# Performance work log

Hardware: AMD Instinct MI355X
Metric: run time of the kernel (lower is better)

The kernel has to match this reference:

```python
import jax, jax.numpy as jnp
import numpy as np

# Dims: lifted grid is N_X x N_Y, input signal has N_IN dims (= N_X*N_Y).
N_X, N_Y, N_IN = 32, 32, 1024
FILT = 33              # resolution-filter taps (odd, centered)
SIGMA0 = 0.1           # resolution_filter_initial_sigma (step 0 of decay schedule)
EPS = 1e-7


def _resolution_filter(sigma):
    # Gaussian taps on normalized coords in ~[-1, 1], normalized to sum 1.
    t = (jnp.arange(FILT, dtype=jnp.float32) - FILT // 2) * (2.0 / FILT)
    k = jnp.exp(-0.5 * jnp.square(t / sigma))
    return k / jnp.sum(k)


def _interpolate_lifting_map(lm_raw, filt):
    # Circular 1-D convolution of the generator parametrization with the
    # Gaussian resolution filter along the input-signal axis.
    P = N_X * N_Y
    pad = FILT // 2
    v = lm_raw.reshape(P, 1, N_IN)
    v = jnp.concatenate([v[..., -pad:], v, v[..., :pad]], axis=-1)  # wrap pad
    k = filt.reshape(1, 1, FILT)
    out = jax.lax.conv_general_dilated(
        v, k, window_strides=(1,), padding='VALID',
        dimension_numbers=('NCH', 'OIH', 'NCH'))
    return out.reshape(N_X, N_Y, N_IN)


def setup_inputs() -> dict:
    key = jax.random.key(0)
    k1, k2 = jax.random.split(key)
    x = jax.random.normal(k1, (16384, N_IN), dtype=jnp.float32)
    lm_raw = jax.random.normal(k2, (N_X, N_Y, N_IN), dtype=jnp.float32) / np.float32(np.sqrt(N_IN))
    return {"x": x, "lm_raw": lm_raw}


def reference(x, lm_raw):
    # _demean_and_normalize_input: per-sample demean + std-normalize.
    mu = jnp.mean(x, axis=-1, keepdims=True)
    sd = jnp.std(x, axis=-1, keepdims=True)
    xn = (x - mu) / (sd + EPS)
    # _sample_resolution_filter + _interpolate_lifting_map
    filt = _resolution_filter(jnp.asarray(SIGMA0, dtype=jnp.float32))
    lm = _interpolate_lifting_map(lm_raw, filt)  # [n_x, n_y, n_in]
    # _lift: y[b, i, j] = sum_n lm[i, j, n] * x[b, n]
    y = jnp.einsum('xyn,bn->bxy', lm, xn)
    return y
```

## Files before the change

### kernel.cpp

```cpp
#include <hip/hip_runtime.h>
#include <hip/hip_bf16.h>

#define N_IN   1024
#define N_P    1024
#define FILT   33
#define PAD    16

typedef __attribute__((ext_vector_type(8))) __bf16 bf16x8;
typedef __attribute__((ext_vector_type(4))) float  f32x4;

#define GLB(p) ((const __attribute__((address_space(1))) unsigned int*)(p))
#define LDSP(p) ((__attribute__((address_space(3))) unsigned int*)(p))

__device__ __forceinline__ unsigned short f2bf(float f) {
    union { __hip_bfloat16 h; unsigned short u; } cv;
    cv.h = __float2bfloat16(f);
    return cv.u;
}

__global__ __launch_bounds__(256)
void normalize_kernel(const float* __restrict__ x, __hip_bfloat16* __restrict__ xn)
{
    const int lane = threadIdx.x & 63;
    const int row  = blockIdx.x * 4 + (threadIdx.x >> 6);

    const float4* xr = reinterpret_cast<const float4*>(x + (size_t)row * N_IN);
    float4 v[4];
    float s = 0.f, s2 = 0.f;
#pragma unroll
    for (int i = 0; i < 4; i++) {
        v[i] = xr[i * 64 + lane];
        s  += v[i].x + v[i].y + v[i].z + v[i].w;
        s2 += v[i].x * v[i].x + v[i].y * v[i].y + v[i].z * v[i].z + v[i].w * v[i].w;
    }
#pragma unroll
    for (int off = 32; off > 0; off >>= 1) {
        s  += __shfl_xor(s,  off, 64);
        s2 += __shfl_xor(s2, off, 64);
    }
    const float mu  = s * (1.0f / N_IN);
    const float var = fmaxf(s2 * (1.0f / N_IN) - mu * mu, 0.0f);
    const float inv = 1.0f / (sqrtf(var) + 1e-7f);

    ushort4* outv = reinterpret_cast<ushort4*>(xn + (size_t)row * N_IN);
#pragma unroll
    for (int i = 0; i < 4; i++) {
        ushort4 o;
        o.x = f2bf((v[i].x - mu) * inv);
        o.y = f2bf((v[i].y - mu) * inv);
        o.z = f2bf((v[i].z - mu) * inv);
        o.w = f2bf((v[i].w - mu) * inv);
        outv[i * 64 + lane] = o;
    }
}

__global__ __launch_bounds__(256)
void conv_kernel(const float* __restrict__ lm_raw, __hip_bfloat16* __restrict__ lm)
{
    __shared__ float row[N_IN];
    __shared__ float fw[FILT];
    const int tid = threadIdx.x;
    const int p   = blockIdx.x;

    if (tid < FILT) {
        float t = (tid - PAD) * (2.0f / FILT);
        float u = t * 10.0f;
        fw[tid] = expf(-0.5f * u * u);
    }
    reinterpret_cast<float4*>(row)[tid] =
        reinterpret_cast<const float4*>(lm_raw + (size_t)p * N_IN)[tid];
    __syncthreads();

    float fsum = 0.f;
#pragma unroll
    for (int f = 0; f < FILT; f++) fsum += fw[f];
    const float inv = 1.0f / fsum;

    const int n0 = tid * 4;
    float o[4] = {0.f, 0.f, 0.f, 0.f};
#pragma unroll
    for (int f = 0; f < FILT; f++) {
        const float w = fw[f];
#pragma unroll
        for (int j = 0; j < 4; j++)
            o[j] += w * row[(n0 + j + f - PAD) & (N_IN - 1)];
    }
    ushort4 ov;
    ov.x = f2bf(o[0] * inv);
    ov.y = f2bf(o[1] * inv);
    ov.z = f2bf(o[2] * inv);
    ov.w = f2bf(o[3] * inv);
    reinterpret_cast<ushort4*>(lm + (size_t)p * N_IN)[tid] = ov;
}

__global__ __launch_bounds__(512, 2)
void gemm_big(const __hip_bfloat16* __restrict__ A,
              const __hip_bfloat16* __restrict__ B,
              float* __restrict__ C,
              int M, int N, int K)
{
    constexpr int BK = 32;
    __shared__ char smem[3][32768];

    const int tid = threadIdx.x;
    const int l   = tid & 63;
    const int w   = tid >> 6;
    const int wm  = w >> 2;
    const int wn  = w & 3;

    const int o    = blockIdx.x;
    const int lin  = (o & 7) * (gridDim.x >> 3) + (o >> 3);
    const int tn   = lin & 3;
    const int tm   = lin >> 2;
    const size_t bm = (size_t)tm * 256;
    const size_t bn = (size_t)tn * 256;

    const int srow = w * 16 + (l >> 2);
    const int scol = 16 * ((l & 3) ^ ((l >> 3) & 3));
    const char* gA = (const char*)(A + (bm + srow) * (size_t)K) + scol;
    const char* gB = (const char*)(B + (bn + srow) * (size_t)K) + scol;
    const size_t rowstep = (size_t)128 * K * 2;

#define STAGE(t, b) do {                                                        \
    const char* a0_ = gA + (size_t)(t) * (BK * 2);                              \
    const char* b0_ = gB + (size_t)(t) * (BK * 2);                              \
    char* La_ = &smem[(b)][0]     + w * 1024;                                   \
    char* Lb_ = &smem[(b)][16384] + w * 1024;                                   \
    __builtin_amdgcn_global_load_lds(GLB(a0_),           LDSP(La_),        16, 0, 0); \
    __builtin_amdgcn_global_load_lds(GLB(a0_ + rowstep), LDSP(La_ + 8192), 16, 0, 0); \
    __builtin_amdgcn_global_load_lds(GLB(b0_),           LDSP(Lb_),        16, 0, 0); \
    __builtin_amdgcn_global_load_lds(GLB(b0_ + rowstep), LDSP(Lb_ + 8192), 16, 0, 0); \
} while (0)

    const int lr = l & 15;
    const int kb = l >> 4;
    const int rslot = 16 * (kb ^ ((lr >> 1) & 3));
    const int abase = (wm * 128 + lr) * 64 + rslot;
    const int bbase = 16384 + (wn * 64 + lr) * 64 + rslot;

    f32x4 acc[8][4] = {};
    const int NT = K / BK;

    STAGE(0, 0);
    STAGE(1, 1);

    int buf = 0;
    for (int t = 0; t < NT; ++t) {
        asm volatile("s_waitcnt lgkmcnt(0)" ::: "memory");
        if (t < NT - 1) asm volatile("s_waitcnt vmcnt(4)" ::: "memory");
        else            asm volatile("s_waitcnt vmcnt(0)" ::: "memory");
        __builtin_amdgcn_s_barrier();
        __builtin_amdgcn_sched_barrier(0);

        {
            const int t2 = t + 2;
            if (t2 < NT) {
                int b2 = buf + 2; if (b2 >= 3) b2 -= 3;
                STAGE(t2, b2);
            }
        }

        const char* Sb = &smem[buf][0];
        bf16x8 bfr[4], afr[4], afr2[4];
#pragma unroll
        for (int n = 0; n < 4; n++) bfr[n]  = *(const bf16x8*)(Sb + bbase + n * 1024);
#pragma unroll
        for (int m = 0; m < 4; m++) afr[m]  = *(const bf16x8*)(Sb + abase + m * 1024);

        __builtin_amdgcn_s_setprio(1);
#pragma unroll
        for (int m = 0; m < 4; m++)
#pragma unroll
            for (int n = 0; n < 4; n++)
                acc[m][n] = __builtin_amdgcn_mfma_f32_16x16x32_bf16(afr[m], bfr[n], acc[m][n], 0, 0, 0);
        __builtin_amdgcn_s_setprio(0);

#pragma unroll
        for (int m = 0; m < 4; m++) afr2[m] = *(const bf16x8*)(Sb + abase + (m + 4) * 1024);

        __builtin_amdgcn_s_setprio(1);
#pragma unroll
        for (int m = 0; m < 4; m++)
#pragma unroll
            for (int n = 0; n < 4; n++)
                acc[m + 4][n] = __builtin_amdgcn_mfma_f32_16x16x32_bf16(afr2[m], bfr[n], acc[m + 4][n], 0, 0, 0);
        __builtin_amdgcn_s_setprio(0);

        if (++buf == 3) buf = 0;
    }
#undef STAGE

    const int crow = (l >> 4) * 4;
    const int ccol = l & 15;
#pragma unroll
    for (int m = 0; m < 8; m++)
#pragma unroll
        for (int n = 0; n < 4; n++) {
#pragma unroll
            for (int r = 0; r < 4; r++) {
                const size_t row = bm + wm * 128 + m * 16 + crow + r;
                const size_t col = bn + wn * 64 + n * 16 + ccol;
                C[row * N + col] = acc[m][n][r];
            }
        }
}

extern "C" void kernel_launch(void* const* d_in, const int* in_sizes, int n_in,
                              void* d_out, int out_size, void* d_ws, size_t ws_size,
                              hipStream_t stream) {
    const float* x      = (const float*)d_in[0];
    const float* lm_raw = (const float*)d_in[1];
    float* out = (float*)d_out;

    const int M = in_sizes[0] / N_IN;

    __hip_bfloat16* xn = (__hip_bfloat16*)d_ws;
    __hip_bfloat16* lm = (__hip_bfloat16*)((char*)d_ws + (size_t)M * N_IN * 2);

    normalize_kernel<<<M / 4, 256, 0, stream>>>(x, xn);
    conv_kernel<<<N_P, 256, 0, stream>>>(lm_raw, lm);

    const int nblk = (M / 256) * (N_P / 256);
    gemm_big<<<nblk, dim3(512), 0, stream>>>(xn, lm, out, M, N_P, N_IN);
}
```

Baseline: 64.65 us.

## Restructure GEMM into 8-phase schedule with BK=64 double-buffered LDS

```diff
diff --git a/kernel.cpp b/kernel.cpp
--- a/kernel.cpp
+++ b/kernel.cpp
@@ -94,13 +94,12 @@
 }
 
 __global__ __launch_bounds__(512, 2)
-void gemm_big(const __hip_bfloat16* __restrict__ A,
+void gemm_8ph(const __hip_bfloat16* __restrict__ A,
               const __hip_bfloat16* __restrict__ B,
               float* __restrict__ C,
               int M, int N, int K)
 {
-    constexpr int BK = 32;
-    __shared__ char smem[3][32768];
+    __shared__ char smem[2][65536];
 
     const int tid = threadIdx.x;
     const int l   = tid & 63;
@@ -115,80 +114,110 @@
     const size_t bm = (size_t)tm * 256;
     const size_t bn = (size_t)tn * 256;
 
-    const int srow = w * 16 + (l >> 2);
-    const int scol = 16 * ((l & 3) ^ ((l >> 3) & 3));
+    const int srow = tid >> 3;
+    const int scol = 16 * ((tid & 7) ^ (srow & 7));
     const char* gA = (const char*)(A + (bm + srow) * (size_t)K) + scol;
     const char* gB = (const char*)(B + (bn + srow) * (size_t)K) + scol;
-    const size_t rowstep = (size_t)128 * K * 2;
-
-#define STAGE(t, b) do {                                                        \
-    const char* a0_ = gA + (size_t)(t) * (BK * 2);                              \
-    const char* b0_ = gB + (size_t)(t) * (BK * 2);                              \
-    char* La_ = &smem[(b)][0]     + w * 1024;                                   \
-    char* Lb_ = &smem[(b)][16384] + w * 1024;                                   \
-    __builtin_amdgcn_global_load_lds(GLB(a0_),           LDSP(La_),        16, 0, 0); \
-    __builtin_amdgcn_global_load_lds(GLB(a0_ + rowstep), LDSP(La_ + 8192), 16, 0, 0); \
-    __builtin_amdgcn_global_load_lds(GLB(b0_),           LDSP(Lb_),        16, 0, 0); \
-    __builtin_amdgcn_global_load_lds(GLB(b0_ + rowstep), LDSP(Lb_ + 8192), 16, 0, 0); \
+    const size_t rowstep = (size_t)64 * K * 2;
+
+#define STAGE8(kt, b) do {                                                            \
+    const char* a_ = gA + (size_t)(kt) * 128;                                         \
+    const char* b_ = gB + (size_t)(kt) * 128;                                         \
+    char* La_ = &smem[(b)][0]     + tid * 16;                                         \
+    char* Lb_ = &smem[(b)][32768] + tid * 16;                                         \
+    __builtin_amdgcn_global_load_lds(GLB(a_),               LDSP(La_),         16, 0, 0); \
+    __builtin_amdgcn_global_load_lds(GLB(a_ + rowstep),     LDSP(La_ + 8192),  16, 0, 0); \
+    __builtin_amdgcn_global_load_lds(GLB(a_ + 2 * rowstep), LDSP(La_ + 16384), 16, 0, 0); \
+    __builtin_amdgcn_global_load_lds(GLB(a_ + 3 * rowstep), LDSP(La_ + 24576), 16, 0, 0); \
+    __builtin_amdgcn_global_load_lds(GLB(b_),               LDSP(Lb_),         16, 0, 0); \
+    __builtin_amdgcn_global_load_lds(GLB(b_ + rowstep),     LDSP(Lb_ + 8192),  16, 0, 0); \
+    __builtin_amdgcn_global_load_lds(GLB(b_ + 2 * rowstep), LDSP(Lb_ + 16384), 16, 0, 0); \
+    __builtin_amdgcn_global_load_lds(GLB(b_ + 3 * rowstep), LDSP(Lb_ + 24576), 16, 0, 0); \
 } while (0)
 
-    const int lr = l & 15;
-    const int kb = l >> 4;
-    const int rslot = 16 * (kb ^ ((lr >> 1) & 3));
-    const int abase = (wm * 128 + lr) * 64 + rslot;
-    const int bbase = 16384 + (wn * 64 + lr) * 64 + rslot;
+#define BAR() do { asm volatile("" ::: "memory");                  \
+                   __builtin_amdgcn_s_barrier();                   \
+                   asm volatile("" ::: "memory"); } while (0)
+#define WAIT_LDS() do { asm volatile("s_waitcnt lgkmcnt(0)" ::: "memory"); \
+                        __builtin_amdgcn_sched_barrier(0); } while (0)
+
+    const int lr   = l & 15;
+    const int kb   = l >> 4;
+    const int akey = lr & 7;
+    const int slot0 = 16 * ((kb)     ^ akey);
+    const int slot1 = 16 * ((4 + kb) ^ akey);
+    const int abase = (wm * 128 + lr) * 128;
+    const int bbase = 32768 + (wn * 64 + lr) * 128;
 
     f32x4 acc[8][4] = {};
-    const int NT = K / BK;
-
-    STAGE(0, 0);
-    STAGE(1, 1);
-
-    int buf = 0;
-    for (int t = 0; t < NT; ++t) {
-        asm volatile("s_waitcnt lgkmcnt(0)" ::: "memory");
-        if (t < NT - 1) asm volatile("s_waitcnt vmcnt(4)" ::: "memory");
-        else            asm volatile("s_waitcnt vmcnt(0)" ::: "memory");
-        __builtin_amdgcn_s_barrier();
-        __builtin_amdgcn_sched_barrier(0);
-
-        {
-            const int t2 = t + 2;
-            if (t2 < NT) {
-                int b2 = buf + 2; if (b2 >= 3) b2 -= 3;
-                STAGE(t2, b2);
-            }
-        }
-
-        const char* Sb = &smem[buf][0];
-        bf16x8 bfr[4], afr[4], afr2[4];
-#pragma unroll
-        for (int n = 0; n < 4; n++) bfr[n]  = *(const bf16x8*)(Sb + bbase + n * 1024);
-#pragma unroll
-        for (int m = 0; m < 4; m++) afr[m]  = *(const bf16x8*)(Sb + abase + m * 1024);
-
-        __builtin_amdgcn_s_setprio(1);
-#pragma unroll
-        for (int m = 0; m < 4; m++)
-#pragma unroll
-            for (int n = 0; n < 4; n++)
-                acc[m][n] = __builtin_amdgcn_mfma_f32_16x16x32_bf16(afr[m], bfr[n], acc[m][n], 0, 0, 0);
-        __builtin_amdgcn_s_setprio(0);
-
-#pragma unroll
-        for (int m = 0; m < 4; m++) afr2[m] = *(const bf16x8*)(Sb + abase + (m + 4) * 1024);
-
-        __builtin_amdgcn_s_setprio(1);
-#pragma unroll
-        for (int m = 0; m < 4; m++)
-#pragma unroll
-            for (int n = 0; n < 4; n++)
-                acc[m + 4][n] = __builtin_amdgcn_mfma_f32_16x16x32_bf16(afr2[m], bfr[n], acc[m + 4][n], 0, 0, 0);
-        __builtin_amdgcn_s_setprio(0);
-
-        if (++buf == 3) buf = 0;
-    }
-#undef STAGE
+    const int NT = K / 64;
+
+    STAGE8(0, 0);
+    asm volatile("s_waitcnt vmcnt(0)" ::: "memory");
+    BAR();
+
+    for (int kt = 0; kt < NT; ++kt) {
+        const int cur = kt & 1;
+        const char* S = &smem[cur][0];
+        bf16x8 bfr0[4], bfr1[4], afr[4];
+
+#pragma unroll
+        for (int n = 0; n < 4; n++) bfr0[n] = *(const bf16x8*)(S + bbase + n * 2048 + slot0);
+#pragma unroll
+        for (int m = 0; m < 4; m++) afr[m]  = *(const bf16x8*)(S + abase + m * 2048 + slot0);
+        if (kt + 1 < NT) STAGE8(kt + 1, cur ^ 1);
+        BAR(); WAIT_LDS();
+        __builtin_amdgcn_s_setprio(1);
+#pragma unroll
+        for (int m = 0; m < 4; m++)
+#pragma unroll
+            for (int n = 0; n < 4; n++)
+                acc[m][n] = __builtin_amdgcn_mfma_f32_16x16x32_bf16(afr[m], bfr0[n], acc[m][n], 0, 0, 0);
+        __builtin_amdgcn_s_setprio(0);
+        BAR();
+
+#pragma unroll
+        for (int m = 0; m < 4; m++) afr[m] = *(const bf16x8*)(S + abase + 8192 + m * 2048 + slot0);
+        BAR(); WAIT_LDS();
+        __builtin_amdgcn_s_setprio(1);
+#pragma unroll
+        for (int m = 0; m < 4; m++)
+#pragma unroll
+            for (int n = 0; n < 4; n++)
+                acc[m + 4][n] = __builtin_amdgcn_mfma_f32_16x16x32_bf16(afr[m], bfr0[n], acc[m + 4][n], 0, 0, 0);
+        __builtin_amdgcn_s_setprio(0);
+        BAR();
+
+#pragma unroll
+        for (int n = 0; n < 4; n++) bfr1[n] = *(const bf16x8*)(S + bbase + n * 2048 + slot1);
+#pragma unroll
+        for (int m = 0; m < 4; m++) afr[m]  = *(const bf16x8*)(S + abase + m * 2048 + slot1);
+        BAR(); WAIT_LDS();
+        __builtin_amdgcn_s_setprio(1);
+#pragma unroll
+        for (int m = 0; m < 4; m++)
+#pragma unroll
+            for (int n = 0; n < 4; n++)
+                acc[m][n] = __builtin_amdgcn_mfma_f32_16x16x32_bf16(afr[m], bfr1[n], acc[m][n], 0, 0, 0);
+        __builtin_amdgcn_s_setprio(0);
+        BAR();
+
+#pragma unroll
+        for (int m = 0; m < 4; m++) afr[m] = *(const bf16x8*)(S + abase + 8192 + m * 2048 + slot1);
+        BAR(); WAIT_LDS();
+        __builtin_amdgcn_s_setprio(1);
+#pragma unroll
+        for (int m = 0; m < 4; m++)
+#pragma unroll
+            for (int n = 0; n < 4; n++)
+                acc[m + 4][n] = __builtin_amdgcn_mfma_f32_16x16x32_bf16(afr[m], bfr1[n], acc[m + 4][n], 0, 0, 0);
+        __builtin_amdgcn_s_setprio(0);
+        asm volatile("s_waitcnt vmcnt(0)" ::: "memory");
+        BAR();
+    }
+#undef STAGE8
+#undef BAR
+#undef WAIT_LDS
 
     const int crow = (l >> 4) * 4;
     const int ccol = l & 15;
@@ -221,5 +250,5 @@
     conv_kernel<<<N_P, 256, 0, stream>>>(lm_raw, lm);
 
     const int nblk = (M / 256) * (N_P / 256);
-    gemm_big<<<nblk, dim3(512), 0, stream>>>(xn, lm, out, M, N_P, N_IN);
-}
+    gemm_8ph<<<nblk, dim3(512), 0, stream>>>(xn, lm, out, M, N_P, N_IN);
+}
```

Result: no change. 64.69 us (+0.1%).

## Load B fragments directly from global into registers, stage only A in LDS

Applied to the files above, without the earlier changes.

```diff
diff --git a/kernel.cpp b/kernel.cpp
--- a/kernel.cpp
+++ b/kernel.cpp
@@ -94,13 +94,13 @@
 }
 
 __global__ __launch_bounds__(512, 2)
-void gemm_big(const __hip_bfloat16* __restrict__ A,
-              const __hip_bfloat16* __restrict__ B,
-              float* __restrict__ C,
-              int M, int N, int K)
+void gemm_breg(const __hip_bfloat16* __restrict__ A,
+               const __hip_bfloat16* __restrict__ B,
+               float* __restrict__ C,
+               int M, int N, int K)
 {
     constexpr int BK = 32;
-    __shared__ char smem[3][32768];
+    __shared__ char As[3][16384];
 
     const int tid = threadIdx.x;
     const int l   = tid & 63;
@@ -118,77 +118,83 @@
     const int srow = w * 16 + (l >> 2);
     const int scol = 16 * ((l & 3) ^ ((l >> 3) & 3));
     const char* gA = (const char*)(A + (bm + srow) * (size_t)K) + scol;
-    const char* gB = (const char*)(B + (bn + srow) * (size_t)K) + scol;
     const size_t rowstep = (size_t)128 * K * 2;
 
-#define STAGE(t, b) do {                                                        \
+#define STAGE_A(t, b) do {                                                      \
     const char* a0_ = gA + (size_t)(t) * (BK * 2);                              \
-    const char* b0_ = gB + (size_t)(t) * (BK * 2);                              \
-    char* La_ = &smem[(b)][0]     + w * 1024;                                   \
-    char* Lb_ = &smem[(b)][16384] + w * 1024;                                   \
+    char* La_ = &As[(b)][0] + w * 1024;                                         \
     __builtin_amdgcn_global_load_lds(GLB(a0_),           LDSP(La_),        16, 0, 0); \
     __builtin_amdgcn_global_load_lds(GLB(a0_ + rowstep), LDSP(La_ + 8192), 16, 0, 0); \
-    __builtin_amdgcn_global_load_lds(GLB(b0_),           LDSP(Lb_),        16, 0, 0); \
-    __builtin_amdgcn_global_load_lds(GLB(b0_ + rowstep), LDSP(Lb_ + 8192), 16, 0, 0); \
 } while (0)
 
     const int lr = l & 15;
     const int kb = l >> 4;
     const int rslot = 16 * (kb ^ ((lr >> 1) & 3));
     const int abase = (wm * 128 + lr) * 64 + rslot;
-    const int bbase = 16384 + (wn * 64 + lr) * 64 + rslot;
+
+    const char* gBr = (const char*)B + ((size_t)(bn + wn * 64 + lr)) * 2048 + kb * 16;
+
+#define LOADB(dst, t) do {                                                      \
+    _Pragma("unroll")                                                           \
+    for (int n_ = 0; n_ < 4; n_++)                                              \
+        dst[n_] = *(const bf16x8*)(gBr + n_ * 32768 + (size_t)(t) * 64);        \
+} while (0)
+
+#define BAR() do { asm volatile("" ::: "memory");                  \
+                   __builtin_amdgcn_s_barrier();                   \
+                   asm volatile("" ::: "memory"); } while (0)
 
     f32x4 acc[8][4] = {};
     const int NT = K / BK;
 
-    STAGE(0, 0);
-    STAGE(1, 1);
-
-    int buf = 0;
-    for (int t = 0; t < NT; ++t) {
+    STAGE_A(0, 0);
+    STAGE_A(1, 1);
+    bf16x8 rB0[4], rB1[4];
+    LOADB(rB0, 0);
+
+    for (int t = 0; t < NT; t += 2) {
         asm volatile("s_waitcnt lgkmcnt(0)" ::: "memory");
-        if (t < NT - 1) asm volatile("s_waitcnt vmcnt(4)" ::: "memory");
-        else            asm volatile("s_waitcnt vmcnt(0)" ::: "memory");
-        __builtin_amdgcn_s_barrier();
-        __builtin_amdgcn_sched_barrier(0);
-
+        asm volatile("s_waitcnt vmcnt(6)" ::: "memory");
+        BAR();
+        if (t + 2 < NT) STAGE_A(t + 2, (t + 2) % 3);
+        LOADB(rB1, t + 1);
         {
-            const int t2 = t + 2;
-            if (t2 < NT) {
-                int b2 = buf + 2; if (b2 >= 3) b2 -= 3;
-                STAGE(t2, b2);
-            }
+            const char* Sa = &As[t % 3][0];
+            bf16x8 afr[8];
+#pragma unroll
+            for (int m = 0; m < 8; m++) afr[m] = *(const bf16x8*)(Sa + abase + m * 1024);
+            __builtin_amdgcn_s_setprio(1);
+#pragma unroll
+            for (int m = 0; m < 8; m++)
+#pragma unroll
+                for (int n = 0; n < 4; n++)
+                    acc[m][n] = __builtin_amdgcn_mfma_f32_16x16x32_bf16(afr[m], rB0[n], acc[m][n], 0, 0, 0);
+            __builtin_amdgcn_s_setprio(0);
         }
 
-        const char* Sb = &smem[buf][0];
-        bf16x8 bfr[4], afr[4], afr2[4];
-#pragma unroll
-        for (int n = 0; n < 4; n++) bfr[n]  = *(const bf16x8*)(Sb + bbase + n * 1024);
-#pragma unroll
-        for (int m = 0; m < 4; m++) afr[m]  = *(const bf16x8*)(Sb + abase + m * 1024);
-
-        __builtin_amdgcn_s_setprio(1);
-#pragma unroll
-        for (int m = 0; m < 4; m++)
-#pragma unroll
-            for (int n = 0; n < 4; n++)
-                acc[m][n] = __builtin_amdgcn_mfma_f32_16x16x32_bf16(afr[m], bfr[n], acc[m][n], 0, 0, 0);
-        __builtin_amdgcn_s_setprio(0);
-
-#pragma unroll
-        for (int m = 0; m < 4; m++) afr2[m] = *(const bf16x8*)(Sb + abase + (m + 4) * 1024);
-
-        __builtin_amdgcn_s_setprio(1);
-#pragma unroll
-        for (int m = 0; m < 4; m++)
-#pragma unroll
-            for (int n = 0; n < 4; n++)
-                acc[m + 4][n] = __builtin_amdgcn_mfma_f32_16x16x32_bf16(afr2[m], bfr[n], acc[m + 4][n], 0, 0, 0);
-        __builtin_amdgcn_s_setprio(0);
-
-        if (++buf == 3) buf = 0;
-    }
-#undef STAGE
+        asm volatile("s_waitcnt lgkmcnt(0)" ::: "memory");
+        if (t + 1 < NT - 1) asm volatile("s_waitcnt vmcnt(6)" ::: "memory");
+        else                asm volatile("s_waitcnt vmcnt(4)" ::: "memory");
+        BAR();
+        if (t + 3 < NT) STAGE_A(t + 3, (t + 3) % 3);
+        if (t + 2 < NT) LOADB(rB0, t + 2);
+        {
+            const char* Sa = &As[(t + 1) % 3][0];
+            bf16x8 afr[8];
+#pragma unroll
+            for (int m = 0; m < 8; m++) afr[m] = *(const bf16x8*)(Sa + abase + m * 1024);
+            __builtin_amdgcn_s_setprio(1);
+#pragma unroll
+            for (int m = 0; m < 8; m++)
+#pragma unroll
+                for (int n = 0; n < 4; n++)
+                    acc[m][n] = __builtin_amdgcn_mfma_f32_16x16x32_bf16(afr[m], rB1[n], acc[m][n], 0, 0, 0);
+            __builtin_amdgcn_s_setprio(0);
+        }
+    }
+#undef STAGE_A
+#undef LOADB
+#undef BAR
 
     const int crow = (l >> 4) * 4;
     const int ccol = l & 15;
@@ -221,5 +227,5 @@
     conv_kernel<<<N_P, 256, 0, stream>>>(lm_raw, lm);
 
     const int nblk = (M / 256) * (N_P / 256);
-    gemm_big<<<nblk, dim3(512), 0, stream>>>(xn, lm, out, M, N_P, N_IN);
-}
+    gemm_breg<<<nblk, dim3(512), 0, stream>>>(xn, lm, out, M, N_P, N_IN);
+}
```

After: 79.21 us. 1.23x slower.
